# Kernel tuning notes

Hardware: AMD Instinct MI355X
Metric: run time of the kernel (lower is better)

Reference implementation:

```python
import jax, jax.numpy as jnp
import numpy as np

EMB = 512
HEADS = 8

def setup_inputs() -> dict:
    key = jax.random.key(0)
    ks = jax.random.split(key, 9)
    s = 1.0 / np.sqrt(EMB)
    x = jax.random.normal(ks[0], (32, 4096, EMB), dtype=jnp.float32)
    Wq = jax.random.normal(ks[1], (EMB, EMB), dtype=jnp.float32) * s
    bq = jax.random.normal(ks[2], (EMB,), dtype=jnp.float32) * s
    Wk = jax.random.normal(ks[3], (EMB, EMB), dtype=jnp.float32) * s
    bk = jax.random.normal(ks[4], (EMB,), dtype=jnp.float32) * s
    Wv = jax.random.normal(ks[5], (EMB, EMB), dtype=jnp.float32) * s
    bv = jax.random.normal(ks[6], (EMB,), dtype=jnp.float32) * s
    Wo = jax.random.normal(ks[7], (EMB, EMB), dtype=jnp.float32) * s
    bo = jax.random.normal(ks[8], (EMB,), dtype=jnp.float32) * s
    return {"x": x, "Wq": Wq, "bq": bq, "Wk": Wk, "bk": bk,
            "Wv": Wv, "bv": bv, "Wo": Wo, "bo": bo}

def reference(x, Wq, bq, Wk, bk, Wv, bv, Wo, bo):
    b, n, e = x.shape
    h = HEADS
    d = e // h
    scale = jnp.asarray(d ** 0.5, x.dtype)
    # torch Linear: y = x @ W.T + b
    q = (x @ Wq.T + bq).reshape(b, n, h, d)
    k = (x @ Wk.T + bk).reshape(b, n, h, d)
    v = (x @ Wv.T + bv).reshape(b, n, h, d)
    # NOTE: contracts over sequence axis n (faithful to original einsum),
    # producing a (b, h, d, d) feature-feature score matrix.
    qk = jnp.einsum('bnhq,bnhk->bhqk', q, k) / scale
    attn = jax.nn.softmax(qk, axis=-1)  # softmax over head_dim axis
    # dropout is identity at inference
    weighted = jnp.einsum('bhqk,bnhk->bnhq', attn, v).reshape(b, n, e)
    return weighted @ Wo.T + bo
```

## Files before the change

### kernel.cpp

```cpp
#include <hip/hip_runtime.h>
#include <hip/hip_bf16.h>
#include <stdint.h>

#define BATCH 32
#define SEQ   4096
#define EMB   512
#define HEADS 8
#define HD    64
#define SCALE 0.125f

typedef __attribute__((ext_vector_type(8))) short bf16x8;
typedef __attribute__((ext_vector_type(4))) float f32x4;

__device__ __forceinline__ unsigned short f2bf(float f) {
    union { float f; unsigned int u; } v; v.f = f;
    unsigned int u = v.u;
    return (unsigned short)((u + 0x7FFFu + ((u >> 16) & 1u)) >> 16);
}
__device__ __forceinline__ float bf2f(unsigned short h) {
    union { unsigned int u; float f; } v; v.u = ((unsigned int)h) << 16;
    return v.f;
}
__device__ __forceinline__ unsigned int cvtpk(float lo, float hi) {
    unsigned int r;
    asm("v_cvt_pk_bf16_f32 %0, %1, %2" : "=v"(r) : "v"(lo), "v"(hi));
    return r;
}
__device__ __forceinline__ float lo_as_f(unsigned int p) {
    union { unsigned int u; float f; } v; v.u = p << 16; return v.f;
}
__device__ __forceinline__ float hi_as_f(unsigned int p) {
    union { unsigned int u; float f; } v; v.u = p & 0xFFFF0000u; return v.f;
}

#define MFMA16(a, b, c) __builtin_amdgcn_mfma_f32_16x16x32_bf16((a), (b), (c), 0, 0, 0)

union F4 { float4 v; float f[4]; };
struct Regs { F4 a0, a1, a2, a3; };

template <int NCHUNK, bool XBF>
__global__ __launch_bounds__(1024) void k1_gram(const float* __restrict__ x,
                                                float* __restrict__ P,
                                                float* __restrict__ svp,
                                                unsigned short* __restrict__ xbf) {
  constexpr int KC  = SEQ / NCHUNK;
  constexpr int NIT = KC / 32;
  constexpr int NWG = BATCH * 4 * NCHUNK;
  constexpr int PER = NWG / 8;
  const int bid = blockIdx.x;
  const int wk  = (bid & 7) * PER + (bid >> 3);
  const int c   = (NCHUNK == 2) ? (wk & 1) : 0;
  const int tt  = (NCHUNK == 2) ? ((wk >> 1) & 3) : (wk & 3);
  const int b   = (NCHUNK == 2) ? (wk >> 3) : (wk >> 2);
  const int mt = (tt >> 1) & 1, nt = tt & 1;
  const int m0 = mt * 256, n0 = nt * 256;
  const bool diag = (mt == nt);
  const float* __restrict__ xb = x + (size_t)b * SEQ * EMB;
  const int kbeg = c * KC;

  __shared__ unsigned short L[2][64 * 148];
  __shared__ float SR[256][8];

  const int tid  = threadIdx.x;
  const int lane = tid & 63;
  const int wave = tid >> 6;
  const int wr = (wave >> 2) * 64;
  const int wc = (wave & 3) * 64;
  const int er  = lane & 15;
  const int kb8 = (lane >> 4) * 8;

  const int fg   = lane;
  const int kgrp = wave >> 1;
  const bool isB = (wave & 1);
  const int pcol = isB ? n0 : m0;
  const bool active = (!diag) || (!isB);

  f32x4 acc[4][4];
#pragma unroll
  for (int i = 0; i < 4; ++i)
#pragma unroll
    for (int j = 0; j < 4; ++j) acc[i][j] = (f32x4){0.f, 0.f, 0.f, 0.f};

  float sacc[4] = {0.f, 0.f, 0.f, 0.f};

  Regs r0;

  auto loadreg = [&](int t) {
    const float* p = &xb[(size_t)(kbeg + t * 32 + kgrp * 4) * EMB + pcol + fg * 4];
    r0.a0.v = *(const float4*)p;
    r0.a1.v = *(const float4*)(p + EMB);
    r0.a2.v = *(const float4*)(p + 2 * EMB);
    r0.a3.v = *(const float4*)(p + 3 * EMB);
  };

  auto stage = [&](int t) {
    unsigned short* __restrict__ Ld = &L[isB ? 1 : 0][0];
#pragma unroll
    for (int i = 0; i < 4; ++i) {
      uint2 w;
      w.x = cvtpk(r0.a0.f[i], r0.a1.f[i]);
      w.y = cvtpk(r0.a2.f[i], r0.a3.f[i]);
      *(uint2*)&Ld[fg * 148 + i * 36 + kgrp * 4] = w;
    }
    if (diag) {
#pragma unroll
      for (int i = 0; i < 4; ++i)
        sacc[i] += (r0.a0.f[i] + r0.a1.f[i]) + (r0.a2.f[i] + r0.a3.f[i]);
      if (XBF) {
        unsigned short* xp = &xbf[((size_t)b * SEQ + kbeg + t * 32 + kgrp * 4) * EMB + m0 + fg * 4];
        uint2 xr;
        xr.x = cvtpk(r0.a0.f[0], r0.a0.f[1]); xr.y = cvtpk(r0.a0.f[2], r0.a0.f[3]);
        *(uint2*)&xp[0] = xr;
        xr.x = cvtpk(r0.a1.f[0], r0.a1.f[1]); xr.y = cvtpk(r0.a1.f[2], r0.a1.f[3]);
        *(uint2*)&xp[EMB] = xr;
        xr.x = cvtpk(r0.a2.f[0], r0.a2.f[1]); xr.y = cvtpk(r0.a2.f[2], r0.a2.f[3]);
        *(uint2*)&xp[2 * EMB] = xr;
        xr.x = cvtpk(r0.a3.f[0], r0.a3.f[1]); xr.y = cvtpk(r0.a3.f[2], r0.a3.f[3]);
        *(uint2*)&xp[3 * EMB] = xr;
      }
    }
  };

  auto frag = [&](const unsigned short* __restrict__ Ls, int e) -> bf16x8 {
    const int off = (e >> 2) * 148 + (e & 3) * 36 + kb8;
    union { bf16x8 v; uint2 u[2]; } r;
    r.u[0] = *(const uint2*)&Ls[off];
    r.u[1] = *(const uint2*)&Ls[off + 4];
    return r.v;
  };

  if (active) loadreg(0);

  for (int it = 0; it < NIT; ++it) {
    __syncthreads();
    if (active) stage(it);
    __syncthreads();
    if (active && (it + 1 < NIT)) loadreg(it + 1);

    const unsigned short* __restrict__ LAs = &L[0][0];
    const unsigned short* __restrict__ LBs = diag ? LAs : &L[1][0];
    bf16x8 bfr[4];
#pragma unroll
    for (int ns = 0; ns < 4; ++ns) bfr[ns] = frag(LBs, wc + ns * 16 + er);
    {
      bf16x8 a0f = frag(LAs, wr + er);
      bf16x8 a1f = frag(LAs, wr + 16 + er);
#pragma unroll
      for (int ns = 0; ns < 4; ++ns) {
        acc[0][ns] = MFMA16(a0f, bfr[ns], acc[0][ns]);
        acc[1][ns] = MFMA16(a1f, bfr[ns], acc[1][ns]);
      }
    }
    {
      bf16x8 a2f = frag(LAs, wr + 32 + er);
      bf16x8 a3f = frag(LAs, wr + 48 + er);
#pragma unroll
      for (int ns = 0; ns < 4; ++ns) {
        acc[2][ns] = MFMA16(a2f, bfr[ns], acc[2][ns]);
        acc[3][ns] = MFMA16(a3f, bfr[ns], acc[3][ns]);
      }
    }
  }

  float* __restrict__ Pc = P + (size_t)(c * BATCH + b) * EMB * EMB;
#pragma unroll
  for (int ms = 0; ms < 4; ++ms)
#pragma unroll
    for (int ns = 0; ns < 4; ++ns)
#pragma unroll
      for (int r = 0; r < 4; ++r) {
        const int row = m0 + wr + ms * 16 + ((lane >> 4) * 4) + r;
        const int col = n0 + wc + ns * 16 + (lane & 15);
        Pc[(size_t)row * EMB + col] = acc[ms][ns][r];
      }

  if (diag) {
    __syncthreads();
    if (!isB) {
#pragma unroll
      for (int i = 0; i < 4; ++i) SR[fg * 4 + i][kgrp] = sacc[i];
    }
    __syncthreads();
    if (tid < 256) {
      float v = 0.f;
#pragma unroll
      for (int j = 0; j < 8; ++j) v += SR[tid][j];
      svp[(size_t)(c * BATCH + b) * EMB + m0 + tid] = v;
    }
  }
}

template <bool TWO>
__global__ __launch_bounds__(256) void k2a_wqg(const float* __restrict__ Wq,
                                               const float* __restrict__ P,
                                               float* __restrict__ A) {
  const int bid = blockIdx.x;
  const int wk  = (bid & 7) * 64 + (bid >> 3);
  const int b  = wk >> 4;
  const int mt = (wk >> 2) & 3;
  const int nt = wk & 3;
  const int m0 = mt * 128, n0 = nt * 128;
  const float* __restrict__ P0b = P + (size_t)b * EMB * EMB;
  const float* __restrict__ P1b = P + (size_t)(BATCH + b) * EMB * EMB;

  __shared__ unsigned short LA[128][40];
  __shared__ unsigned short LBhi[128][40];
  __shared__ unsigned short LBlo[128][40];

  const int tid  = threadIdx.x;
  const int lane = tid & 63;
  const int wave = tid >> 6;
  const int wr = (wave >> 1) * 64;
  const int wc = (wave & 1) * 64;

  f32x4 acc[4][4];
#pragma unroll
  for (int i = 0; i < 4; ++i)
#pragma unroll
    for (int j = 0; j < 4; ++j) acc[i][j] = (f32x4){0.f, 0.f, 0.f, 0.f};

  const int rA = tid >> 3, fgA = tid & 7;

  for (int k0 = 0; k0 < EMB; k0 += 32) {
    __syncthreads();
#pragma unroll
    for (int it = 0; it < 4; ++it) {
      const int r = rA + it * 32;
      const float4 v = *(const float4*)&Wq[(size_t)(m0 + r) * EMB + k0 + fgA * 4];
      uint2 u; u.x = cvtpk(v.x, v.y); u.y = cvtpk(v.z, v.w);
      *(uint2*)&LA[r][fgA * 4] = u;
    }
#pragma unroll
    for (int it = 0; it < 4; ++it) {
      const int r = rA + it * 32;
      float4 v = *(const float4*)&P0b[(size_t)(n0 + r) * EMB + k0 + fgA * 4];
      if (TWO) {
        const float4 v1 = *(const float4*)&P1b[(size_t)(n0 + r) * EMB + k0 + fgA * 4];
        v.x += v1.x; v.y += v1.y; v.z += v1.z; v.w += v1.w;
      }
      uint2 h; h.x = cvtpk(v.x, v.y); h.y = cvtpk(v.z, v.w);
      uint2 l;
      l.x = cvtpk(v.x - lo_as_f(h.x), v.y - hi_as_f(h.x));
      l.y = cvtpk(v.z - lo_as_f(h.y), v.w - hi_as_f(h.y));
      *(uint2*)&LBhi[r][fgA * 4] = h;
      *(uint2*)&LBlo[r][fgA * 4] = l;
    }
    __syncthreads();
    bf16x8 af[4], bh[4], bl[4];
#pragma unroll
    for (int ms = 0; ms < 4; ++ms)
      af[ms] = *(const bf16x8*)&LA[wr + ms*16 + (lane & 15)][(lane >> 4) * 8];
#pragma unroll
    for (int ns = 0; ns < 4; ++ns) {
      bh[ns] = *(const bf16x8*)&LBhi[wc + ns*16 + (lane & 15)][(lane >> 4) * 8];
      bl[ns] = *(const bf16x8*)&LBlo[wc + ns*16 + (lane & 15)][(lane >> 4) * 8];
    }
#pragma unroll
    for (int ms = 0; ms < 4; ++ms)
#pragma unroll
      for (int ns = 0; ns < 4; ++ns) {
        acc[ms][ns] = MFMA16(af[ms], bh[ns], acc[ms][ns]);
        acc[ms][ns] = MFMA16(af[ms], bl[ns], acc[ms][ns]);
      }
  }

  float* __restrict__ Ab = A + (size_t)b * EMB * EMB;
#pragma unroll
  for (int ms = 0; ms < 4; ++ms)
#pragma unroll
    for (int ns = 0; ns < 4; ++ns)
#pragma unroll
      for (int r = 0; r < 4; ++r) {
        const int row = m0 + wr + ms*16 + ((lane >> 4) * 4) + r;
        const int col = n0 + wc + ns*16 + (lane & 15);
        Ab[(size_t)row * EMB + col] = acc[ms][ns][r];
      }
}

template <int NCHUNK>
__global__ __launch_bounds__(256) void k2b_logits(const float* __restrict__ A,
                                                  const float* __restrict__ Wq,
                                                  const float* __restrict__ Wk,
                                                  const float* __restrict__ bq,
                                                  const float* __restrict__ bk,
                                                  const float* __restrict__ svp,
                                                  unsigned short* __restrict__ attn) {
  const int blk = blockIdx.x;
  const int b = blk >> 3;
  const int h = blk & 7;
  const float* __restrict__ Ab = A + (size_t)b * EMB * EMB + (size_t)h * HD * EMB;

  __shared__ unsigned short LAhi[64][40];
  __shared__ unsigned short LAlo[64][40];
  __shared__ unsigned short LB[64][40];
  __shared__ float U[HD], W[HD];

  const int tid  = threadIdx.x;
  const int lane = tid & 63;
  const int wave = tid >> 6;

  if (tid < 128) {
    const int q = tid & 63;
    const float* __restrict__ wrow = (tid < 64 ? Wq : Wk) + (size_t)(h * HD + q) * EMB;
    float a = 0.f;
    for (int i = 0; i < EMB; i += 4) {
      const float4 wv = *(const float4*)&wrow[i];
      float4 sv = *(const float4*)&svp[(size_t)b * EMB + i];
      if (NCHUNK == 2) {
        const float4 s1 = *(const float4*)&svp[(size_t)(BATCH + b) * EMB + i];
        sv.x += s1.x; sv.y += s1.y; sv.z += s1.z; sv.w += s1.w;
      }
      a += wv.x*sv.x + wv.y*sv.y + wv.z*sv.z + wv.w*sv.w;
    }
    if (tid < 64) U[q] = a; else W[q] = a;
  }

  f32x4 acc[4];
#pragma unroll
  for (int i = 0; i < 4; ++i) acc[i] = (f32x4){0.f, 0.f, 0.f, 0.f};

  const int r8 = tid >> 3, fg8 = tid & 7;

  for (int k0 = 0; k0 < EMB; k0 += 32) {
    __syncthreads();
#pragma unroll
    for (int it = 0; it < 2; ++it) {
      const int r = r8 + it * 32;
      const float4 v = *(const float4*)&Ab[(size_t)r * EMB + k0 + fg8 * 4];
      uint2 h2; h2.x = cvtpk(v.x, v.y); h2.y = cvtpk(v.z, v.w);
      uint2 l2;
      l2.x = cvtpk(v.x - lo_as_f(h2.x), v.y - hi_as_f(h2.x));
      l2.y = cvtpk(v.z - lo_as_f(h2.y), v.w - hi_as_f(h2.y));
      *(ushort4*)&LAhi[r][fg8*4] = *(ushort4*)&h2;
      *(ushort4*)&LAlo[r][fg8*4] = *(ushort4*)&l2;
      const float4 wv = *(const float4*)&Wk[(size_t)(h*HD + r) * EMB + k0 + fg8 * 4];
      uint2 ub; ub.x = cvtpk(wv.x, wv.y); ub.y = cvtpk(wv.z, wv.w);
      *(ushort4*)&LB[r][fg8*4] = *(ushort4*)&ub;
    }
    __syncthreads();
    const bf16x8 ah = *(const bf16x8*)&LAhi[wave*16 + (lane & 15)][(lane >> 4) * 8];
    const bf16x8 al = *(const bf16x8*)&LAlo[wave*16 + (lane & 15)][(lane >> 4) * 8];
#pragma unroll
    for (int ns = 0; ns < 4; ++ns) {
      const bf16x8 bb = *(const bf16x8*)&LB[ns*16 + (lane & 15)][(lane >> 4) * 8];
      acc[ns] = MFMA16(ah, bb, acc[ns]);
      acc[ns] = MFMA16(al, bb, acc[ns]);
    }
  }

  const int colb = lane & 15;
  float bkv[4], wv_[4];
#pragma unroll
  for (int ns = 0; ns < 4; ++ns) {
    bkv[ns] = bk[h*HD + ns*16 + colb];
    wv_[ns] = W[ns*16 + colb];
  }
  unsigned short* __restrict__ ab = attn + (size_t)(b * HEADS + h) * HD * HD;
#pragma unroll
  for (int r = 0; r < 4; ++r) {
    const int row = wave*16 + ((lane >> 4) * 4) + r;
    const float bqv = bq[h*HD + row];
    const float uv  = U[row];
    float vals[4];
#pragma unroll
    for (int ns = 0; ns < 4; ++ns)
      vals[ns] = (acc[ns][r] + uv * bkv[ns] + bqv * wv_[ns] + 4096.f * bqv * bkv[ns]) * SCALE;
    float mx = fmaxf(fmaxf(vals[0], vals[1]), fmaxf(vals[2], vals[3]));
#pragma unroll
    for (int m = 1; m < 16; m <<= 1) mx = fmaxf(mx, __shfl_xor(mx, m));
    float sum = 0.f;
#pragma unroll
    for (int ns = 0; ns < 4; ++ns) { vals[ns] = expf(vals[ns] - mx); sum += vals[ns]; }
#pragma unroll
    for (int m = 1; m < 16; m <<= 1) sum += __shfl_xor(sum, m);
    const float inv = 1.f / sum;
#pragma unroll
    for (int ns = 0; ns < 4; ++ns)
      ab[(size_t)row * HD + ns*16 + colb] = f2bf(vals[ns] * inv);
  }
}

__global__ __launch_bounds__(256) void k3a_c(const float* __restrict__ Wo,
                                             const unsigned short* __restrict__ attn,
                                             unsigned short* __restrict__ C) {
  const int blk = blockIdx.x;
  const int b  = blk >> 5;
  const int h  = (blk >> 2) & 7;
  const int mt = blk & 3;
  const int m0 = mt * 128;

  __shared__ unsigned short LA[128][72];
  __shared__ unsigned short LB[64][72];

  const int tid  = threadIdx.x;
  const int lane = tid & 63;
  const int wave = tid >> 6;

  {
    const int r  = tid >> 4;
    const int fg = tid & 15;
#pragma unroll
    for (int it = 0; it < 8; ++it) {
      const int rr = r + it * 16;
      const float4 v = *(const float4*)&Wo[(size_t)(m0 + rr) * EMB + h*HD + fg * 4];
      uint2 u; u.x = cvtpk(v.x, v.y); u.y = cvtpk(v.z, v.w);
      *(uint2*)&LA[rr][fg * 4] = u;
    }
  }
  {
    const unsigned short* __restrict__ ab = attn + (size_t)(b * HEADS + h) * HD * HD;
#pragma unroll
    for (int it = 0; it < 16; ++it) {
      const int f  = tid + 256 * it;
      const int q  = f >> 6;
      const int kp = f & 63;
      LB[kp][q] = ab[q * HD + kp];
    }
  }
  __syncthreads();

  f32x4 acc[2][4];
#pragma unroll
  for (int i = 0; i < 2; ++i)
#pragma unroll
    for (int j = 0; j < 4; ++j) acc[i][j] = (f32x4){0.f, 0.f, 0.f, 0.f};

#pragma unroll
  for (int kk = 0; kk < 2; ++kk) {
    bf16x8 af[2], bfr[4];
#pragma unroll
    for (int ms = 0; ms < 2; ++ms)
      af[ms] = *(const bf16x8*)&LA[wave*32 + ms*16 + (lane & 15)][kk*32 + (lane >> 4) * 8];
#pragma unroll
    for (int ns = 0; ns < 4; ++ns)
      bfr[ns] = *(const bf16x8*)&LB[ns*16 + (lane & 15)][kk*32 + (lane >> 4) * 8];
#pragma unroll
    for (int ms = 0; ms < 2; ++ms)
#pragma unroll
      for (int ns = 0; ns < 4; ++ns)
        acc[ms][ns] = MFMA16(af[ms], bfr[ns], acc[ms][ns]);
  }

  unsigned short* __restrict__ Cb = C + (size_t)b * EMB * EMB;
#pragma unroll
  for (int ms = 0; ms < 2; ++ms)
#pragma unroll
    for (int ns = 0; ns < 4; ++ns)
#pragma unroll
      for (int r = 0; r < 4; ++r) {
        const int row = m0 + wave*32 + ms*16 + ((lane >> 4) * 4) + r;
        const int col = h*HD + ns*16 + (lane & 15);
        Cb[(size_t)row * EMB + col] = f2bf(acc[ms][ns][r]);
      }
}

__global__ __launch_bounds__(256) void k3b_d(const unsigned short* __restrict__ C,
                                             const float* __restrict__ Wv,
                                             unsigned short* __restrict__ D) {
  const int bid = blockIdx.x;
  const int wk  = (bid & 7) * 64 + (bid >> 3);
  const int b  = wk >> 4;
  const int mt = (wk >> 2) & 3;
  const int nt = wk & 3;
  const int m0 = mt * 128, n0 = nt * 128;
  const unsigned short* __restrict__ Cb = C + (size_t)b * EMB * EMB;

  __shared__ unsigned short LA[128][40];
  __shared__ unsigned short LB[32 * 148];

  const int tid  = threadIdx.x;
  const int lane = tid & 63;
  const int wave = tid >> 6;
  const int wr = (wave >> 1) * 64;
  const int wc = (wave & 1) * 64;
  const int er  = lane & 15;
  const int kb8 = (lane >> 4) * 8;

  f32x4 acc[4][4];
#pragma unroll
  for (int i = 0; i < 4; ++i)
#pragma unroll
    for (int j = 0; j < 4; ++j) acc[i][j] = (f32x4){0.f, 0.f, 0.f, 0.f};

  const int rA = tid >> 3, fgA = tid & 7;
  const int fgB = tid & 31;
  const int kgB = tid >> 5;

  for (int k0 = 0; k0 < EMB; k0 += 32) {
    __syncthreads();
#pragma unroll
    for (int it = 0; it < 4; ++it) {
      const int r = rA + it * 32;
      *(ushort4*)&LA[r][fgA*4] = *(const ushort4*)&Cb[(size_t)(m0 + r) * EMB + k0 + fgA * 4];
    }
    {
      const float* p = &Wv[(size_t)(k0 + kgB * 4) * EMB + n0 + fgB * 4];
      F4 b0, b1, b2, b3;
      b0.v = *(const float4*)p;
      b1.v = *(const float4*)(p + EMB);
      b2.v = *(const float4*)(p + 2 * EMB);
      b3.v = *(const float4*)(p + 3 * EMB);
#pragma unroll
      for (int i = 0; i < 4; ++i) {
        uint2 w;
        w.x = cvtpk(b0.f[i], b1.f[i]);
        w.y = cvtpk(b2.f[i], b3.f[i]);
        *(uint2*)&LB[fgB * 148 + i * 36 + kgB * 4] = w;
      }
    }
    __syncthreads();
    bf16x8 af[4], bfr[4];
#pragma unroll
    for (int ms = 0; ms < 4; ++ms)
      af[ms] = *(const bf16x8*)&LA[wr + ms*16 + er][kb8];
#pragma unroll
    for (int ns = 0; ns < 4; ++ns) {
      const int e = wc + ns * 16 + er;
      const int off = (e >> 2) * 148 + (e & 3) * 36 + kb8;
      union { bf16x8 v; uint2 u[2]; } r;
      r.u[0] = *(const uint2*)&LB[off];
      r.u[1] = *(const uint2*)&LB[off + 4];
      bfr[ns] = r.v;
    }
#pragma unroll
    for (int ms = 0; ms < 4; ++ms)
#pragma unroll
      for (int ns = 0; ns < 4; ++ns)
        acc[ms][ns] = MFMA16(af[ms], bfr[ns], acc[ms][ns]);
  }

  unsigned short* __restrict__ Db = D + (size_t)b * EMB * EMB;
#pragma unroll
  for (int ms = 0; ms < 4; ++ms)
#pragma unroll
    for (int ns = 0; ns < 4; ++ns)
#pragma unroll
      for (int r = 0; r < 4; ++r) {
        const int row = m0 + wr + ms*16 + ((lane >> 4) * 4) + r;
        const int col = n0 + wc + ns*16 + (lane & 15);
        Db[(size_t)row * EMB + col] = f2bf(acc[ms][ns][r]);
      }
}

__global__ __launch_bounds__(256) void k3c_e(const unsigned short* __restrict__ C,
                                             const float* __restrict__ bv,
                                             const float* __restrict__ bo,
                                             float* __restrict__ evec) {
  const int blk = blockIdx.x;
  const int b = blk >> 4;
  const int g = blk & 15;
  const int tid  = threadIdx.x;
  const int lane = tid & 63;
  const int wave = tid >> 6;

  __shared__ float BV[EMB];
  for (int i = tid; i < EMB; i += 256) BV[i] = bv[i];
  __syncthreads();

  const unsigned short* __restrict__ Cb = C + (size_t)b * EMB * EMB;
#pragma unroll
  for (int p = 0; p < 8; ++p) {
    const int row = g*32 + wave*8 + p;
    const unsigned short* cr = &Cb[(size_t)row * EMB + lane * 8];
    const float* bvp = &BV[lane * 8];
    ushort4 v0 = *(const ushort4*)&cr[0];
    ushort4 v1 = *(const ushort4*)&cr[4];
    float a = bf2f(v0.x)*bvp[0] + bf2f(v0.y)*bvp[1] + bf2f(v0.z)*bvp[2] + bf2f(v0.w)*bvp[3]
            + bf2f(v1.x)*bvp[4] + bf2f(v1.y)*bvp[5] + bf2f(v1.z)*bvp[6] + bf2f(v1.w)*bvp[7];
#pragma unroll
    for (int m = 1; m < 64; m <<= 1) a += __shfl_xor(a, m);
    if (lane == 0) evec[b * EMB + row] = a + bo[row];
  }
}

template <bool XBF>
__global__ __launch_bounds__(1024) void k4_out(const float* __restrict__ x,
                                               const unsigned short* __restrict__ xbf,
                                               const unsigned short* __restrict__ D,
                                               const float* __restrict__ evec,
                                               float* __restrict__ out) {
  const int bid = blockIdx.x;
  const int wk  = (bid & 7) * 128 + (bid >> 3);
  const int b  = wk >> 5;
  const int mt = wk & 31;
  const int m0 = mt * 128;
  const float* __restrict__ xb = x + (size_t)b * SEQ * EMB;
  const unsigned short* __restrict__ xbb = xbf + (size_t)b * SEQ * EMB;
  const unsigned short* __restrict__ Db = D + (size_t)b * EMB * EMB;

  __shared__ unsigned short LA[128 * 40];
  __shared__ unsigned short LB[512 * 40];

  const int tid  = threadIdx.x;
  const int lane = tid & 63;
  const int wave = tid >> 6;
  const int wr = (wave >> 3) * 64;
  const int wc = (wave & 7) * 64;
  const int er  = lane & 15;
  const int kb8 = (lane >> 4) * 8;

  const int rsA = tid >> 3;
  const int kgA = tid & 7;
  const int rsB = tid >> 1;
  const int kgB = (tid & 1) * 16;

  f32x4 acc[4][4];
#pragma unroll
  for (int i = 0; i < 4; ++i)
#pragma unroll
    for (int j = 0; j < 4; ++j) acc[i][j] = (f32x4){0.f, 0.f, 0.f, 0.f};

  uint2 ua;
  F4 fa;
  uint4 ub0, ub1;

  auto loadreg = [&](int k0) {
    if (XBF) {
      ua = *(const uint2*)&xbb[(size_t)(m0 + rsA) * EMB + k0 + kgA * 4];
    } else {
      fa.v = *(const float4*)&xb[(size_t)(m0 + rsA) * EMB + k0 + kgA * 4];
    }
    ub0 = *(const uint4*)&Db[(size_t)rsB * EMB + k0 + kgB];
    ub1 = *(const uint4*)&Db[(size_t)rsB * EMB + k0 + kgB + 8];
  };

  auto stage = [&]() {
    if (XBF) {
      *(uint2*)&LA[rsA * 40 + kgA * 4] = ua;
    } else {
      uint2 w; w.x = cvtpk(fa.f[0], fa.f[1]); w.y = cvtpk(fa.f[2], fa.f[3]);
      *(uint2*)&LA[rsA * 40 + kgA * 4] = w;
    }
    *(uint4*)&LB[rsB * 40 + kgB] = ub0;
    *(uint4*)&LB[rsB * 40 + kgB + 8] = ub1;
  };

  loadreg(0);

  for (int it = 0; it < 16; ++it) {
    __syncthreads();
    stage();
    __syncthreads();
    if (it + 1 < 16) loadreg((it + 1) * 32);

    bf16x8 bfr[4];
#pragma unroll
    for (int ns = 0; ns < 4; ++ns)
      bfr[ns] = *(const bf16x8*)&LB[(wc + ns * 16 + er) * 40 + kb8];
    {
      bf16x8 a0f = *(const bf16x8*)&LA[(wr + er) * 40 + kb8];
      bf16x8 a1f = *(const bf16x8*)&LA[(wr + 16 + er) * 40 + kb8];
#pragma unroll
      for (int ns = 0; ns < 4; ++ns) {
        acc[0][ns] = MFMA16(a0f, bfr[ns], acc[0][ns]);
        acc[1][ns] = MFMA16(a1f, bfr[ns], acc[1][ns]);
      }
    }
    {
      bf16x8 a2f = *(const bf16x8*)&LA[(wr + 32 + er) * 40 + kb8];
      bf16x8 a3f = *(const bf16x8*)&LA[(wr + 48 + er) * 40 + kb8];
#pragma unroll
      for (int ns = 0; ns < 4; ++ns) {
        acc[2][ns] = MFMA16(a2f, bfr[ns], acc[2][ns]);
        acc[3][ns] = MFMA16(a3f, bfr[ns], acc[3][ns]);
      }
    }
  }

  float ev4[4];
#pragma unroll
  for (int ns = 0; ns < 4; ++ns)
    ev4[ns] = evec[b * EMB + wc + ns * 16 + (lane & 15)];

#pragma unroll
  for (int ms = 0; ms < 4; ++ms)
#pragma unroll
    for (int ns = 0; ns < 4; ++ns)
#pragma unroll
      for (int r = 0; r < 4; ++r) {
        const int row = m0 + wr + ms * 16 + ((lane >> 4) * 4) + r;
        const int col = wc + ns * 16 + (lane & 15);
        out[((size_t)b * SEQ + row) * EMB + col] = acc[ms][ns][r] + ev4[ns];
      }
}

extern "C" void kernel_launch(void* const* d_in, const int* in_sizes, int n_in,
                              void* d_out, int out_size, void* d_ws, size_t ws_size,
                              hipStream_t stream) {
  (void)in_sizes; (void)n_in; (void)out_size;
  const float* x  = (const float*)d_in[0];
  const float* Wq = (const float*)d_in[1];
  const float* bq = (const float*)d_in[2];
  const float* Wk = (const float*)d_in[3];
  const float* bk = (const float*)d_in[4];
  const float* Wv = (const float*)d_in[5];
  const float* bv = (const float*)d_in[6];
  const float* Wo = (const float*)d_in[7];
  const float* bo = (const float*)d_in[8];
  float* out = (float*)d_out;

  char* ws = (char*)d_ws;
  const size_t MB = (size_t)1 << 20;
  const size_t XBF_BYTES = (size_t)BATCH * SEQ * EMB * 2;
  const size_t NEED2 = XBF_BYTES + 98 * MB + 256 * 1024;
  const size_t NEED1 = XBF_BYTES + 66 * MB + 256 * 1024;

  if (ws_size >= NEED2) {
    unsigned short* xbf  = (unsigned short*)(ws);
    float*          P    = (float*)(ws + XBF_BYTES);
    unsigned short* Cm   = (unsigned short*)(ws + XBF_BYTES);
    unsigned short* Dm   = (unsigned short*)(ws + XBF_BYTES + 16 * MB);
    float*          A    = (float*)(ws + XBF_BYTES + 64 * MB);
    unsigned short* attn = (unsigned short*)(ws + XBF_BYTES + 96 * MB);
    float*          svp  = (float*)(ws + XBF_BYTES + 98 * MB);
    float*          ev   = (float*)(ws + XBF_BYTES + 98 * MB + 192 * 1024);

    hipLaunchKernelGGL((k1_gram<2, true>), dim3(BATCH * 8),  dim3(1024), 0, stream, x, P, svp, xbf);
    hipLaunchKernelGGL((k2a_wqg<true>),    dim3(BATCH * 16), dim3(256), 0, stream, Wq, P, A);
    hipLaunchKernelGGL((k2b_logits<2>),    dim3(BATCH * 8),  dim3(256), 0, stream, A, Wq, Wk, bq, bk, svp, attn);
    hipLaunchKernelGGL(k3a_c,              dim3(BATCH * 32), dim3(256), 0, stream, Wo, attn, Cm);
    hipLaunchKernelGGL(k3b_d,              dim3(BATCH * 16), dim3(256), 0, stream, Cm, Wv, Dm);
    hipLaunchKernelGGL(k3c_e,              dim3(BATCH * 16), dim3(256), 0, stream, Cm, bv, bo, ev);
    hipLaunchKernelGGL((k4_out<true>),     dim3(BATCH * 32), dim3(1024), 0, stream, x, xbf, Dm, ev, out);
  } else if (ws_size >= NEED1) {
    unsigned short* xbf  = (unsigned short*)(ws);
    float*          P    = (float*)(ws + XBF_BYTES);
    unsigned short* Cm   = (unsigned short*)(ws + XBF_BYTES);
    unsigned short* Dm   = (unsigned short*)(ws + XBF_BYTES + 16 * MB);
    float*          A    = (float*)(ws + XBF_BYTES + 32 * MB);
    unsigned short* attn = (unsigned short*)(ws + XBF_BYTES + 64 * MB);
    float*          svp  = (float*)(ws + XBF_BYTES + 66 * MB);
    float*          ev   = (float*)(ws + XBF_BYTES + 66 * MB + 192 * 1024);

    hipLaunchKernelGGL((k1_gram<1, true>), dim3(BATCH * 4),  dim3(1024), 0, stream, x, P, svp, xbf);
    hipLaunchKernelGGL((k2a_wqg<false>),   dim3(BATCH * 16), dim3(256), 0, stream, Wq, P, A);
    hipLaunchKernelGGL((k2b_logits<1>),    dim3(BATCH * 8),  dim3(256), 0, stream, A, Wq, Wk, bq, bk, svp, attn);
    hipLaunchKernelGGL(k3a_c,              dim3(BATCH * 32), dim3(256), 0, stream, Wo, attn, Cm);
    hipLaunchKernelGGL(k3b_d,              dim3(BATCH * 16), dim3(256), 0, stream, Cm, Wv, Dm);
    hipLaunchKernelGGL(k3c_e,              dim3(BATCH * 16), dim3(256), 0, stream, Cm, bv, bo, ev);
    hipLaunchKernelGGL((k4_out<true>),     dim3(BATCH * 32), dim3(1024), 0, stream, x, xbf, Dm, ev, out);
  } else {
    unsigned short* xbf  = (unsigned short*)(ws);
    float*          P    = (float*)(ws);
    unsigned short* Cm   = (unsigned short*)(ws);
    unsigned short* Dm   = (unsigned short*)(ws + 16 * MB);
    float*          A    = (float*)(ws + 32 * MB);
    unsigned short* attn = (unsigned short*)(ws + 64 * MB);
    float*          svp  = (float*)(ws + 66 * MB);
    float*          ev   = (float*)(ws + 66 * MB + 192 * 1024);

    hipLaunchKernelGGL((k1_gram<1, false>), dim3(BATCH * 4),  dim3(1024), 0, stream, x, P, svp, xbf);
    hipLaunchKernelGGL((k2a_wqg<false>),    dim3(BATCH * 16), dim3(256), 0, stream, Wq, P, A);
    hipLaunchKernelGGL((k2b_logits<1>),     dim3(BATCH * 8),  dim3(256), 0, stream, A, Wq, Wk, bq, bk, svp, attn);
    hipLaunchKernelGGL(k3a_c,               dim3(BATCH * 32), dim3(256), 0, stream, Wo, attn, Cm);
    hipLaunchKernelGGL(k3b_d,               dim3(BATCH * 16), dim3(256), 0, stream, Cm, Wv, Dm);
    hipLaunchKernelGGL(k3c_e,               dim3(BATCH * 16), dim3(256), 0, stream, Cm, bv, bo, ev);
    hipLaunchKernelGGL((k4_out<false>),     dim3(BATCH * 32), dim3(1024), 0, stream, x, xbf, Dm, ev, out);
  }
}
```

Before: 363.2 us.

## Enlarge k2a tile to 256x128 with 1024 threads and register prefetch

The Wq·P GEMM kernel now uses 1024-thread blocks computing 256x128 tiles, with each wave owning a 64x32 subtile. Global loads for the next k-slice are issued into registers before the current slice's MFMAs run, so load latency overlaps compute. The block-to-work mapping of both k2a and k2b is interleaved so consecutive blocks spread across batches. This roughly halves the repeated P staging and bf16 hi/lo splitting per output, but leaves fewer blocks and more registers per block, which may reduce occupancy.

Result: slower. 372.1 us (+2.5%).

```diff
diff --git a/kernel.cpp b/kernel.cpp
--- a/kernel.cpp
+++ b/kernel.cpp
@@ -191,74 +191,87 @@
 }
 
 template <bool TWO>
-__global__ __launch_bounds__(256) void k2a_wqg(const float* __restrict__ Wq,
-                                               const float* __restrict__ P,
-                                               float* __restrict__ A) {
+__global__ __launch_bounds__(1024) void k2a_wqg(const float* __restrict__ Wq,
+                                                const float* __restrict__ P,
+                                                float* __restrict__ A) {
   const int bid = blockIdx.x;
-  const int wk  = (bid & 7) * 64 + (bid >> 3);
-  const int b  = wk >> 4;
-  const int mt = (wk >> 2) & 3;
+  const int wk  = (bid & 7) * 32 + (bid >> 3);
+  const int b  = wk >> 3;
+  const int mt = (wk >> 2) & 1;
   const int nt = wk & 3;
-  const int m0 = mt * 128, n0 = nt * 128;
+  const int m0 = mt * 256, n0 = nt * 128;
   const float* __restrict__ P0b = P + (size_t)b * EMB * EMB;
   const float* __restrict__ P1b = P + (size_t)(BATCH + b) * EMB * EMB;
 
-  __shared__ unsigned short LA[128][40];
-  __shared__ unsigned short LBhi[128][40];
-  __shared__ unsigned short LBlo[128][40];
+  __shared__ unsigned short LA[256 * 40];
+  __shared__ unsigned short LBhi[128 * 40];
+  __shared__ unsigned short LBlo[128 * 40];
 
   const int tid  = threadIdx.x;
   const int lane = tid & 63;
   const int wave = tid >> 6;
-  const int wr = (wave >> 1) * 64;
-  const int wc = (wave & 1) * 64;
-
-  f32x4 acc[4][4];
+  const int wr = (wave >> 2) * 64;
+  const int wc = (wave & 3) * 32;
+  const int er  = lane & 15;
+  const int kb8 = (lane >> 4) * 8;
+
+  const int rsA = tid >> 2;
+  const int kgA = (tid & 3) * 8;
+  const int rsB = tid >> 3;
+  const int kgB = (tid & 7) * 4;
+
+  f32x4 acc[4][2];
 #pragma unroll
   for (int i = 0; i < 4; ++i)
 #pragma unroll
-    for (int j = 0; j < 4; ++j) acc[i][j] = (f32x4){0.f, 0.f, 0.f, 0.f};
-
-  const int rA = tid >> 3, fgA = tid & 7;
-
-  for (int k0 = 0; k0 < EMB; k0 += 32) {
-    __syncthreads();
-#pragma unroll
-    for (int it = 0; it < 4; ++it) {
-      const int r = rA + it * 32;
-      const float4 v = *(const float4*)&Wq[(size_t)(m0 + r) * EMB + k0 + fgA * 4];
-      uint2 u; u.x = cvtpk(v.x, v.y); u.y = cvtpk(v.z, v.w);
-      *(uint2*)&LA[r][fgA * 4] = u;
-    }
-#pragma unroll
-    for (int it = 0; it < 4; ++it) {
-      const int r = rA + it * 32;
-      float4 v = *(const float4*)&P0b[(size_t)(n0 + r) * EMB + k0 + fgA * 4];
-      if (TWO) {
-        const float4 v1 = *(const float4*)&P1b[(size_t)(n0 + r) * EMB + k0 + fgA * 4];
-        v.x += v1.x; v.y += v1.y; v.z += v1.z; v.w += v1.w;
-      }
-      uint2 h; h.x = cvtpk(v.x, v.y); h.y = cvtpk(v.z, v.w);
-      uint2 l;
-      l.x = cvtpk(v.x - lo_as_f(h.x), v.y - hi_as_f(h.x));
-      l.y = cvtpk(v.z - lo_as_f(h.y), v.w - hi_as_f(h.y));
-      *(uint2*)&LBhi[r][fgA * 4] = h;
-      *(uint2*)&LBlo[r][fgA * 4] = l;
-    }
-    __syncthreads();
-    bf16x8 af[4], bh[4], bl[4];
+    for (int j = 0; j < 2; ++j) acc[i][j] = (f32x4){0.f, 0.f, 0.f, 0.f};
+
+  F4 ra0, ra1, rb0, rb1;
+
+  auto loadreg = [&](int k0) {
+    const float* pa = &Wq[(size_t)(m0 + rsA) * EMB + k0 + kgA];
+    ra0.v = *(const float4*)pa;
+    ra1.v = *(const float4*)(pa + 4);
+    rb0.v = *(const float4*)&P0b[(size_t)(n0 + rsB) * EMB + k0 + kgB];
+    if (TWO) rb1.v = *(const float4*)&P1b[(size_t)(n0 + rsB) * EMB + k0 + kgB];
+  };
+
+  auto stage = [&]() {
+    uint4 wa;
+    wa.x = cvtpk(ra0.f[0], ra0.f[1]); wa.y = cvtpk(ra0.f[2], ra0.f[3]);
+    wa.z = cvtpk(ra1.f[0], ra1.f[1]); wa.w = cvtpk(ra1.f[2], ra1.f[3]);
+    *(uint4*)&LA[rsA * 40 + kgA] = wa;
+    float v0 = rb0.f[0], v1 = rb0.f[1], v2 = rb0.f[2], v3 = rb0.f[3];
+    if (TWO) { v0 += rb1.f[0]; v1 += rb1.f[1]; v2 += rb1.f[2]; v3 += rb1.f[3]; }
+    uint2 h; h.x = cvtpk(v0, v1); h.y = cvtpk(v2, v3);
+    uint2 l;
+    l.x = cvtpk(v0 - lo_as_f(h.x), v1 - hi_as_f(h.x));
+    l.y = cvtpk(v2 - lo_as_f(h.y), v3 - hi_as_f(h.y));
+    *(uint2*)&LBhi[rsB * 40 + kgB] = h;
+    *(uint2*)&LBlo[rsB * 40 + kgB] = l;
+  };
+
+  loadreg(0);
+
+  for (int it = 0; it < 16; ++it) {
+    __syncthreads();
+    stage();
+    __syncthreads();
+    if (it + 1 < 16) loadreg((it + 1) * 32);
+
+    bf16x8 af[4], bh[2], bl[2];
 #pragma unroll
     for (int ms = 0; ms < 4; ++ms)
-      af[ms] = *(const bf16x8*)&LA[wr + ms*16 + (lane & 15)][(lane >> 4) * 8];
-#pragma unroll
-    for (int ns = 0; ns < 4; ++ns) {
-      bh[ns] = *(const bf16x8*)&LBhi[wc + ns*16 + (lane & 15)][(lane >> 4) * 8];
-      bl[ns] = *(const bf16x8*)&LBlo[wc + ns*16 + (lane & 15)][(lane >> 4) * 8];
+      af[ms] = *(const bf16x8*)&LA[(wr + ms * 16 + er) * 40 + kb8];
+#pragma unroll
+    for (int ns = 0; ns < 2; ++ns) {
+      bh[ns] = *(const bf16x8*)&LBhi[(wc + ns * 16 + er) * 40 + kb8];
+      bl[ns] = *(const bf16x8*)&LBlo[(wc + ns * 16 + er) * 40 + kb8];
     }
 #pragma unroll
     for (int ms = 0; ms < 4; ++ms)
 #pragma unroll
-      for (int ns = 0; ns < 4; ++ns) {
+      for (int ns = 0; ns < 2; ++ns) {
         acc[ms][ns] = MFMA16(af[ms], bh[ns], acc[ms][ns]);
         acc[ms][ns] = MFMA16(af[ms], bl[ns], acc[ms][ns]);
       }
@@ -268,11 +281,11 @@
 #pragma unroll
   for (int ms = 0; ms < 4; ++ms)
 #pragma unroll
-    for (int ns = 0; ns < 4; ++ns)
+    for (int ns = 0; ns < 2; ++ns)
 #pragma unroll
       for (int r = 0; r < 4; ++r) {
-        const int row = m0 + wr + ms*16 + ((lane >> 4) * 4) + r;
-        const int col = n0 + wc + ns*16 + (lane & 15);
+        const int row = m0 + wr + ms * 16 + ((lane >> 4) * 4) + r;
+        const int col = n0 + wc + ns * 16 + (lane & 15);
         Ab[(size_t)row * EMB + col] = acc[ms][ns][r];
       }
 }
@@ -285,9 +298,10 @@
                                                   const float* __restrict__ bk,
                                                   const float* __restrict__ svp,
                                                   unsigned short* __restrict__ attn) {
-  const int blk = blockIdx.x;
-  const int b = blk >> 3;
-  const int h = blk & 7;
+  const int bid = blockIdx.x;
+  const int wk  = (bid & 7) * 32 + (bid >> 3);
+  const int b = wk >> 3;
+  const int h = wk & 7;
   const float* __restrict__ Ab = A + (size_t)b * EMB * EMB + (size_t)h * HD * EMB;
 
   __shared__ unsigned short LAhi[64][40];
@@ -716,7 +730,7 @@
     float*          ev   = (float*)(ws + XBF_BYTES + 98 * MB + 192 * 1024);
 
     hipLaunchKernelGGL((k1_gram<2, true>), dim3(BATCH * 8),  dim3(1024), 0, stream, x, P, svp, xbf);
-    hipLaunchKernelGGL((k2a_wqg<true>),    dim3(BATCH * 16), dim3(256), 0, stream, Wq, P, A);
+    hipLaunchKernelGGL((k2a_wqg<true>),    dim3(BATCH * 8),  dim3(1024), 0, stream, Wq, P, A);
     hipLaunchKernelGGL((k2b_logits<2>),    dim3(BATCH * 8),  dim3(256), 0, stream, A, Wq, Wk, bq, bk, svp, attn);
     hipLaunchKernelGGL(k3a_c,              dim3(BATCH * 32), dim3(256), 0, stream, Wo, attn, Cm);
     hipLaunchKernelGGL(k3b_d,              dim3(BATCH * 16), dim3(256), 0, stream, Cm, Wv, Dm);
@@ -733,7 +747,7 @@
     float*          ev   = (float*)(ws + XBF_BYTES + 66 * MB + 192 * 1024);
 
     hipLaunchKernelGGL((k1_gram<1, true>), dim3(BATCH * 4),  dim3(1024), 0, stream, x, P, svp, xbf);
-    hipLaunchKernelGGL((k2a_wqg<false>),   dim3(BATCH * 16), dim3(256), 0, stream, Wq, P, A);
+    hipLaunchKernelGGL((k2a_wqg<false>),   dim3(BATCH * 8),  dim3(1024), 0, stream, Wq, P, A);
     hipLaunchKernelGGL((k2b_logits<1>),    dim3(BATCH * 8),  dim3(256), 0, stream, A, Wq, Wk, bq, bk, svp, attn);
     hipLaunchKernelGGL(k3a_c,              dim3(BATCH * 32), dim3(256), 0, stream, Wo, attn, Cm);
     hipLaunchKernelGGL(k3b_d,              dim3(BATCH * 16), dim3(256), 0, stream, Cm, Wv, Dm);
@@ -750,7 +764,7 @@
     float*          ev   = (float*)(ws + 66 * MB + 192 * 1024);
 
     hipLaunchKernelGGL((k1_gram<1, false>), dim3(BATCH * 4),  dim3(1024), 0, stream, x, P, svp, xbf);
-    hipLaunchKernelGGL((k2a_wqg<false>),    dim3(BATCH * 16), dim3(256), 0, stream, Wq, P, A);
+    hipLaunchKernelGGL((k2a_wqg<false>),    dim3(BATCH * 8),  dim3(1024), 0, stream, Wq, P, A);
     hipLaunchKernelGGL((k2b_logits<1>),     dim3(BATCH * 8),  dim3(256), 0, stream, A, Wq, Wk, bq, bk, svp, attn);
     hipLaunchKernelGGL(k3a_c,               dim3(BATCH * 32), dim3(256), 0, stream, Wo, attn, Cm);
     hipLaunchKernelGGL(k3b_d,               dim3(BATCH * 16), dim3(256), 0, stream, Cm, Wv, Dm);
```
